# Kernel optimization log

Measured on AMD Instinct MI355X. Metric: run time of the kernel, lower is better.

Reference implementation:

```python
import jax, jax.numpy as jnp
import numpy as np

B, L, H, N, O = 64, 512, 768, 50, 768
ALPHA = 0.3  # leaky relu slope in GAT
NEG_INF = -9e15


def _position_encoding(n, d):
    # standard sinusoidal PE, shape [n, d]
    pos = jnp.arange(n, dtype=jnp.float32)[:, None]              # [n,1]
    div = jnp.exp(jnp.arange(0, d, 2, dtype=jnp.float32) * (-np.log(10000.0) / d))  # [d/2]
    ang = pos * div[None, :]                                     # [n, d/2]
    return jnp.stack([jnp.sin(ang), jnp.cos(ang)], axis=-1).reshape(n, d)


def _gat_layer(x, adj, W, b, a, ab):
    # Dense GAT layer. Original builds an [N,N,2F] concat tensor then applies
    # linear a; mathematically identical to splitting a into src/dst halves.
    Wh = x @ W + b                                               # [N,F]
    Fdim = Wh.shape[-1]
    a_src = Wh @ a[:Fdim]                                        # [N]
    a_dst = Wh @ a[Fdim:]                                        # [N]
    e = jax.nn.leaky_relu(a_src[:, None] + a_dst[None, :] + ab, negative_slope=ALPHA)
    att = jax.nn.softmax(jnp.where(adj > 0, e, NEG_INF), axis=1)  # rows sum to 1
    return att @ Wh                                              # [N,F]


def setup_inputs() -> dict:
    key = jax.random.key(0)
    ks = jax.random.split(key, 16)
    s = 1.0 / np.sqrt(H)
    utter_embedding = jax.random.normal(ks[0], (B, L, H), jnp.float32)
    cls_ids = jnp.sort(jax.random.randint(ks[1], (B, N), 0, L), axis=1).astype(jnp.int32)
    adj = jax.random.randint(ks[2], (B, N, N), 0, 2).astype(jnp.int32)
    adj = adj | jnp.eye(N, dtype=jnp.int32)  # ensure self loops so softmax rows are valid
    return {
        "utter_embedding": utter_embedding,
        "cls_ids": cls_ids,
        "adj": adj,
        # GAT head 0 (concat=True)
        "W1": jax.random.normal(ks[3], (H, H), jnp.float32) * s,
        "b1": jnp.zeros((H,), jnp.float32),
        "a1": jax.random.normal(ks[4], (2 * H,), jnp.float32) * s,
        "ab1": jnp.zeros((), jnp.float32),
        # GAT out layer (concat=False)
        "W2": jax.random.normal(ks[5], (H, H), jnp.float32) * s,
        "b2": jnp.zeros((H,), jnp.float32),
        "a2": jax.random.normal(ks[6], (2 * H,), jnp.float32) * s,
        "ab2": jnp.zeros((), jnp.float32),
        # Attention pooling over utterances
        "Wa": jax.random.normal(ks[7], (H, H), jnp.float32) * s,
        "ba": jnp.zeros((H,), jnp.float32),
        "v": jax.random.normal(ks[8], (H,), jnp.float32) * s,
        # Final linear
        "Wl": jax.random.normal(ks[9], (H, O), jnp.float32) * s,
        "bl": jnp.zeros((O,), jnp.float32),
    }


def reference(utter_embedding, cls_ids, adj, W1, b1, a1, ab1, W2, b2, a2, ab2,
              Wa, ba, v, Wl, bl):
    pe = _position_encoding(N, H)                                # [N,H]

    def per_dialogue(emb, ids, A):
        # gather [CLS] utterance embeddings: index_select
        x = jnp.take(emb, ids, axis=0)                           # [N,H]
        x = x + pe                                               # position encoder
        # GAT: 1 head concat -> elu, out layer -> elu, residual
        h = jax.nn.elu(_gat_layer(x, A, W1, b1, a1, ab1))
        h = jax.nn.elu(_gat_layer(h, A, W2, b2, a2, ab2)) + x    # residual per GAT.forward
        # attention pooling over N utterances
        scores = jax.nn.softmax(jnp.tanh(h @ Wa + ba) @ v, axis=0)  # [N]
        return scores @ h                                        # [H]

    dialogue = jax.vmap(per_dialogue)(utter_embedding, cls_ids, adj)  # [B,H]
    return dialogue @ Wl + bl                                    # [B,O]
```

## Files before the change

### kernel.cpp

```cpp
#include <hip/hip_runtime.h>
#include <hip/hip_bf16.h>
#include <math.h>

typedef __attribute__((ext_vector_type(8))) short bf16x8;
typedef __attribute__((ext_vector_type(4))) float f32x4;

constexpr int Bn = 64;
constexpr int Ln = 512;
constexpr int Hd = 768;
constexpr int Nn = 50;
constexpr int On = 768;

struct PrepArgs {
  const float* src[4];
  __hip_bfloat16* dst[4];
  float* aux;
  int auxn;
};

__global__ __launch_bounds__(256) void prep_kernel(PrepArgs args) {
  int job = blockIdx.y;
  if (job < 4) {
    __shared__ float tile[32][33];
    int t = blockIdx.x;
    int bx = (t % 24) * 32, by = (t / 24) * 32;
    const float* W = args.src[job];
    __hip_bfloat16* Wt = args.dst[job];
    int c = threadIdx.x & 31, r0 = threadIdx.x >> 5;
    for (int r = r0; r < 32; r += 8)
      tile[r][c] = W[(size_t)(bx + r) * Hd + by + c];
    __syncthreads();
    for (int r = r0; r < 32; r += 8)
      Wt[(size_t)(by + r) * Hd + bx + c] = __float2bfloat16(tile[c][r]);
  } else {
    int idx = blockIdx.x * 256 + threadIdx.x;
    if (idx < args.auxn) args.aux[idx] = 0.f;
  }
}

__global__ __launch_bounds__(256) void gather_pe_kernel(
    const float* __restrict__ emb, const int* __restrict__ ids,
    float* __restrict__ xf, __hip_bfloat16* __restrict__ xb) {
  int bn = blockIdx.x;
  int b = bn / Nn, n = bn % Nn;
  int id = ids[bn];
  const float* src = emb + ((size_t)b * Ln + id) * Hd;
  float* xo = xf + (size_t)bn * Hd;
  __hip_bfloat16* xbo = xb + (size_t)bn * Hd;
  const float kLog = 9.210340371976184f / (float)Hd;
  for (int h = threadIdx.x; h < Hd; h += 256) {
    int he = h & ~1;
    float freq = expf(-(float)he * kLog);
    float ang = (float)n * freq;
    float pe = (h & 1) ? cosf(ang) : sinf(ang);
    float v = src[h] + pe;
    xo[h] = v;
    xbo[h] = __float2bfloat16(v);
  }
}

template <int EPI>
__global__ __launch_bounds__(256) void gemm_kernel(
    const __hip_bfloat16* __restrict__ A, const __hip_bfloat16* __restrict__ Bt,
    const float* __restrict__ bias, float* __restrict__ C,
    const float* __restrict__ avec, float* __restrict__ o1,
    float* __restrict__ o2) {
  __shared__ __hip_bfloat16 As[64][40];
  __shared__ __hip_bfloat16 Bs[64][40];
  int tid = threadIdx.x;
  int wave = tid >> 6, lane = tid & 63;
  int lr = lane & 15, lq = lane >> 4;
  int row0 = blockIdx.x * 64, col0 = blockIdx.y * 64;
  int sr = tid >> 2, sk = (tid & 3) * 8;
  const __hip_bfloat16* Ap = A + (size_t)(row0 + sr) * Hd + sk;
  const __hip_bfloat16* Bp = Bt + (size_t)(col0 + sr) * Hd + sk;
  f32x4 acc[4] = {};
  for (int kt = 0; kt < Hd; kt += 32) {
    *(uint4*)&As[sr][sk] = *(const uint4*)(Ap + kt);
    *(uint4*)&Bs[sr][sk] = *(const uint4*)(Bp + kt);
    __syncthreads();
    bf16x8 af = *(const bf16x8*)&As[wave * 16 + lr][lq * 8];
#pragma unroll
    for (int ct = 0; ct < 4; ++ct) {
      bf16x8 bfrag = *(const bf16x8*)&Bs[ct * 16 + lr][lq * 8];
      acc[ct] = __builtin_amdgcn_mfma_f32_16x16x32_bf16(af, bfrag, acc[ct], 0, 0, 0);
    }
    __syncthreads();
  }
  int cr0 = row0 + wave * 16 + lq * 4;
  if (EPI == 0) {
    float ps[4] = {}, pd[4] = {};
#pragma unroll
    for (int ct = 0; ct < 4; ++ct) {
      int gc = col0 + ct * 16 + lr;
      float bv = bias[gc];
      float as_ = avec[gc], ad_ = avec[Hd + gc];
#pragma unroll
      for (int r = 0; r < 4; ++r) {
        float v = acc[ct][r] + bv;
        C[(size_t)(cr0 + r) * Hd + gc] = v;
        ps[r] += v * as_;
        pd[r] += v * ad_;
      }
    }
#pragma unroll
    for (int off = 8; off; off >>= 1)
#pragma unroll
      for (int r = 0; r < 4; ++r) {
        ps[r] += __shfl_xor(ps[r], off);
        pd[r] += __shfl_xor(pd[r], off);
      }
    if (lr == 0)
#pragma unroll
      for (int r = 0; r < 4; ++r) {
        atomicAdd(&o1[cr0 + r], ps[r]);
        atomicAdd(&o2[cr0 + r], pd[r]);
      }
  } else {
    float pr[4] = {};
#pragma unroll
    for (int ct = 0; ct < 4; ++ct) {
      int gc = col0 + ct * 16 + lr;
      float bv = bias[gc];
      float vv_ = avec[gc];
#pragma unroll
      for (int r = 0; r < 4; ++r) {
        float t = tanhf(acc[ct][r] + bv);
        pr[r] += t * vv_;
      }
    }
#pragma unroll
    for (int off = 8; off; off >>= 1)
#pragma unroll
      for (int r = 0; r < 4; ++r) pr[r] += __shfl_xor(pr[r], off);
    if (lr == 0)
#pragma unroll
      for (int r = 0; r < 4; ++r) atomicAdd(&o1[cr0 + r], pr[r]);
  }
}

template <int LAYER>
__global__ __launch_bounds__(256) void attf_kernel(
    const float* __restrict__ ssrc, const float* __restrict__ sdst,
    const int* __restrict__ adj, const float* __restrict__ ab,
    const float* __restrict__ Wh, const float* __restrict__ xres,
    float* __restrict__ hf, __hip_bfloat16* __restrict__ hb) {
  int b = blockIdx.y, h0 = blockIdx.x * 128;
  __shared__ float attL[Nn * Nn];
  float abv = ab[0];
  for (int idx = threadIdx.x; idx < Nn * Nn; idx += 256) {
    int i = idx / Nn, j = idx - i * Nn;
    float t = ssrc[b * Nn + i] + sdst[b * Nn + j] + abv;
    t = t > 0.f ? t : 0.3f * t;
    attL[idx] = (adj[(size_t)b * Nn * Nn + idx] > 0) ? t : -9.0e15f;
  }
  __syncthreads();
  if (threadIdx.x < Nn) {
    int i = threadIdx.x;
    float m = -3.0e38f;
    for (int j = 0; j < Nn; ++j) m = fmaxf(m, attL[i * Nn + j]);
    float s = 0.f;
    for (int j = 0; j < Nn; ++j) {
      float p = expf(attL[i * Nn + j] - m);
      attL[i * Nn + j] = p;
      s += p;
    }
    float inv = 1.f / s;
    for (int j = 0; j < Nn; ++j) attL[i * Nn + j] *= inv;
  }
  __syncthreads();
  int col = threadIdx.x & 127, half = threadIdx.x >> 7;
  int i0 = half * 25;
  float acc[25] = {};
  const float* Whb = Wh + ((size_t)b * Nn) * Hd + h0 + col;
  for (int j = 0; j < Nn; j += 2) {
    float w0 = Whb[(size_t)j * Hd];
    float w1 = Whb[(size_t)(j + 1) * Hd];
#pragma unroll
    for (int ii = 0; ii < 25; ++ii) {
      float2 a2 = *(const float2*)&attL[(i0 + ii) * Nn + j];
      acc[ii] += a2.x * w0 + a2.y * w1;
    }
  }
#pragma unroll
  for (int ii = 0; ii < 25; ++ii) {
    float v = acc[ii];
    v = v > 0.f ? v : expf(v) - 1.f;
    size_t off = ((size_t)b * Nn + i0 + ii) * Hd + h0 + col;
    if (LAYER == 2) {
      v += xres[off];
      hf[off] = v;
    }
    hb[off] = __float2bfloat16(v);
  }
}

__global__ __launch_bounds__(256) void poolfinal_kernel(
    const float* __restrict__ sraw, const float* __restrict__ h2,
    const __hip_bfloat16* __restrict__ Wlt, const float* __restrict__ bl,
    float* __restrict__ out) {
  int b = blockIdx.x;
  __shared__ float sc[Nn];
  __shared__ float ds[Hd];
  if (threadIdx.x < 64) {
    int j = threadIdx.x;
    float e = (j < Nn) ? sraw[b * Nn + j] : -3.0e38f;
    float m = e;
#pragma unroll
    for (int off = 32; off; off >>= 1) m = fmaxf(m, __shfl_xor(m, off));
    float p = (j < Nn) ? expf(e - m) : 0.f;
    float s = p;
#pragma unroll
    for (int off = 32; off; off >>= 1) s += __shfl_xor(s, off);
    if (j < Nn) sc[j] = p / s;
  }
  __syncthreads();
  for (int h = threadIdx.x; h < Hd; h += 256) {
    float a = 0.f;
#pragma unroll 10
    for (int j = 0; j < Nn; ++j) a += sc[j] * h2[((size_t)b * Nn + j) * Hd + h];
    ds[h] = a;
  }
  __syncthreads();
  for (int oo = 0; oo < 3; ++oo) {
    int o = oo * 256 + threadIdx.x;
    float acc = bl[o];
    const uint4* wr = (const uint4*)(Wlt + (size_t)o * Hd);
    for (int kk = 0; kk < Hd / 8; ++kk) {
      union { uint4 u; unsigned short s[8]; } w;
      w.u = wr[kk];
#pragma unroll
      for (int t = 0; t < 8; ++t)
        acc += ds[kk * 8 + t] * __uint_as_float((unsigned)w.s[t] << 16);
    }
    out[(size_t)b * On + o] = acc;
  }
}

extern "C" void kernel_launch(void* const* d_in, const int* in_sizes, int n_in,
                              void* d_out, int out_size, void* d_ws, size_t ws_size,
                              hipStream_t stream) {
  const float* emb = (const float*)d_in[0];
  const int* ids = (const int*)d_in[1];
  const int* adj = (const int*)d_in[2];
  const float* W1 = (const float*)d_in[3];
  const float* b1 = (const float*)d_in[4];
  const float* a1 = (const float*)d_in[5];
  const float* ab1 = (const float*)d_in[6];
  const float* W2 = (const float*)d_in[7];
  const float* b2 = (const float*)d_in[8];
  const float* a2 = (const float*)d_in[9];
  const float* ab2 = (const float*)d_in[10];
  const float* Wa = (const float*)d_in[11];
  const float* ba = (const float*)d_in[12];
  const float* vv = (const float*)d_in[13];
  const float* Wl = (const float*)d_in[14];
  const float* bl = (const float*)d_in[15];
  float* out = (float*)d_out;

  char* p = (char*)d_ws;
  auto alloc = [&](size_t bytes) {
    char* r = p;
    p += (bytes + 255) & ~(size_t)255;
    return r;
  };
  __hip_bfloat16* Wt1 = (__hip_bfloat16*)alloc((size_t)Hd * Hd * 2);
  __hip_bfloat16* Wt2 = (__hip_bfloat16*)alloc((size_t)Hd * Hd * 2);
  __hip_bfloat16* Wta = (__hip_bfloat16*)alloc((size_t)Hd * Hd * 2);
  __hip_bfloat16* Wlt = (__hip_bfloat16*)alloc((size_t)Hd * On * 2);
  float* aux = (float*)alloc(5 * Bn * Nn * 4);
  float* ssrc1 = aux;
  float* sdst1 = aux + Bn * Nn;
  float* ssrc2 = aux + 2 * Bn * Nn;
  float* sdst2 = aux + 3 * Bn * Nn;
  float* sraw = aux + 4 * Bn * Nn;
  float* xf = (float*)alloc((size_t)Bn * Nn * Hd * 4);
  __hip_bfloat16* xb = (__hip_bfloat16*)alloc((size_t)Bn * Nn * Hd * 2);
  float* Wh = (float*)alloc((size_t)Bn * Nn * Hd * 4);
  float* h2f = (float*)alloc((size_t)Bn * Nn * Hd * 4);
  __hip_bfloat16* hb = (__hip_bfloat16*)alloc((size_t)Bn * Nn * Hd * 2);

  PrepArgs pa;
  pa.src[0] = W1; pa.src[1] = W2; pa.src[2] = Wa; pa.src[3] = Wl;
  pa.dst[0] = Wt1; pa.dst[1] = Wt2; pa.dst[2] = Wta; pa.dst[3] = Wlt;
  pa.aux = aux; pa.auxn = 5 * Bn * Nn;
  prep_kernel<<<dim3(576, 5), 256, 0, stream>>>(pa);

  gather_pe_kernel<<<Bn * Nn, 256, 0, stream>>>(emb, ids, xf, xb);

  dim3 ggrid(Bn * Nn / 64, Hd / 64);
  dim3 agrid(Hd / 128, Bn);

  gemm_kernel<0><<<ggrid, 256, 0, stream>>>(xb, Wt1, b1, Wh, a1, ssrc1, sdst1);
  attf_kernel<1><<<agrid, 256, 0, stream>>>(ssrc1, sdst1, adj, ab1, Wh,
                                            nullptr, nullptr, hb);
  gemm_kernel<0><<<ggrid, 256, 0, stream>>>(hb, Wt2, b2, Wh, a2, ssrc2, sdst2);
  attf_kernel<2><<<agrid, 256, 0, stream>>>(ssrc2, sdst2, adj, ab2, Wh,
                                            xf, h2f, hb);
  gemm_kernel<1><<<ggrid, 256, 0, stream>>>(hb, Wta, ba, nullptr, vv, sraw,
                                            nullptr);
  poolfinal_kernel<<<Bn, 256, 0, stream>>>(sraw, h2f, Wlt, bl, out);
}
```

Baseline: 313.3 us.

## Double-buffer GEMM LDS, store Wh in bf16, merge gather into prep kernel

The GEMM main loop now uses two LDS buffers. The next k-tile is loaded into registers while MFMAs run on the current tile, which removes one barrier per iteration. The intermediate Wh is stored as bf16 instead of fp32, halving its write and read traffic in the GEMM epilogue and the attention kernel, at some precision cost. The gather/position-encoding kernel is folded into the prep kernel to save one launch, and the attention grid is flattened to 1D.

```diff
diff --git a/kernel.cpp b/kernel.cpp
--- a/kernel.cpp
+++ b/kernel.cpp
@@ -14,59 +14,59 @@
 struct PrepArgs {
   const float* src[4];
   __hip_bfloat16* dst[4];
+  const float* emb;
+  const int* ids;
+  float* xf;
+  __hip_bfloat16* xb;
   float* aux;
   int auxn;
 };
 
-__global__ __launch_bounds__(256) void prep_kernel(PrepArgs args) {
-  int job = blockIdx.y;
-  if (job < 4) {
-    __shared__ float tile[32][33];
-    int t = blockIdx.x;
-    int bx = (t % 24) * 32, by = (t / 24) * 32;
-    const float* W = args.src[job];
-    __hip_bfloat16* Wt = args.dst[job];
+__global__ __launch_bounds__(256) void prep_kernel(PrepArgs a) {
+  __shared__ float tile[32][33];
+  int bx = blockIdx.x;
+  if (bx < 2304) {
+    int job = bx / 576, t = bx % 576;
+    const float* W = a.src[job];
+    __hip_bfloat16* Wt = a.dst[job];
+    int tx = (t % 24) * 32, ty = (t / 24) * 32;
     int c = threadIdx.x & 31, r0 = threadIdx.x >> 5;
     for (int r = r0; r < 32; r += 8)
-      tile[r][c] = W[(size_t)(bx + r) * Hd + by + c];
+      tile[r][c] = W[(size_t)(tx + r) * Hd + ty + c];
     __syncthreads();
     for (int r = r0; r < 32; r += 8)
-      Wt[(size_t)(by + r) * Hd + bx + c] = __float2bfloat16(tile[c][r]);
+      Wt[(size_t)(ty + r) * Hd + tx + c] = __float2bfloat16(tile[c][r]);
+  } else if (bx < 5504) {
+    int bn = bx - 2304;
+    int b = bn / Nn, n = bn % Nn;
+    int id = a.ids[bn];
+    const float* src = a.emb + ((size_t)b * Ln + id) * Hd;
+    float* xo = a.xf + (size_t)bn * Hd;
+    __hip_bfloat16* xbo = a.xb + (size_t)bn * Hd;
+    const float kLog = 9.210340371976184f / (float)Hd;
+    for (int h = threadIdx.x; h < Hd; h += 256) {
+      int he = h & ~1;
+      float freq = expf(-(float)he * kLog);
+      float ang = (float)n * freq;
+      float pe = (h & 1) ? cosf(ang) : sinf(ang);
+      float v = src[h] + pe;
+      xo[h] = v;
+      xbo[h] = __float2bfloat16(v);
+    }
   } else {
-    int idx = blockIdx.x * 256 + threadIdx.x;
-    if (idx < args.auxn) args.aux[idx] = 0.f;
-  }
-}
-
-__global__ __launch_bounds__(256) void gather_pe_kernel(
-    const float* __restrict__ emb, const int* __restrict__ ids,
-    float* __restrict__ xf, __hip_bfloat16* __restrict__ xb) {
-  int bn = blockIdx.x;
-  int b = bn / Nn, n = bn % Nn;
-  int id = ids[bn];
-  const float* src = emb + ((size_t)b * Ln + id) * Hd;
-  float* xo = xf + (size_t)bn * Hd;
-  __hip_bfloat16* xbo = xb + (size_t)bn * Hd;
-  const float kLog = 9.210340371976184f / (float)Hd;
-  for (int h = threadIdx.x; h < Hd; h += 256) {
-    int he = h & ~1;
-    float freq = expf(-(float)he * kLog);
-    float ang = (float)n * freq;
-    float pe = (h & 1) ? cosf(ang) : sinf(ang);
-    float v = src[h] + pe;
-    xo[h] = v;
-    xbo[h] = __float2bfloat16(v);
+    int idx = (bx - 5504) * 256 + threadIdx.x;
+    if (idx < a.auxn) a.aux[idx] = 0.f;
   }
 }
 
 template <int EPI>
 __global__ __launch_bounds__(256) void gemm_kernel(
     const __hip_bfloat16* __restrict__ A, const __hip_bfloat16* __restrict__ Bt,
-    const float* __restrict__ bias, float* __restrict__ C,
+    const float* __restrict__ bias, __hip_bfloat16* __restrict__ C,
     const float* __restrict__ avec, float* __restrict__ o1,
     float* __restrict__ o2) {
-  __shared__ __hip_bfloat16 As[64][40];
-  __shared__ __hip_bfloat16 Bs[64][40];
+  __shared__ __hip_bfloat16 As[2][64][40];
+  __shared__ __hip_bfloat16 Bs[2][64][40];
   int tid = threadIdx.x;
   int wave = tid >> 6, lane = tid & 63;
   int lr = lane & 15, lq = lane >> 4;
@@ -74,18 +74,34 @@
   int sr = tid >> 2, sk = (tid & 3) * 8;
   const __hip_bfloat16* Ap = A + (size_t)(row0 + sr) * Hd + sk;
   const __hip_bfloat16* Bp = Bt + (size_t)(col0 + sr) * Hd + sk;
+  uint4 ra = *(const uint4*)Ap;
+  uint4 rb = *(const uint4*)Bp;
+  *(uint4*)&As[0][sr][sk] = ra;
+  *(uint4*)&Bs[0][sr][sk] = rb;
   f32x4 acc[4] = {};
-  for (int kt = 0; kt < Hd; kt += 32) {
-    *(uint4*)&As[sr][sk] = *(const uint4*)(Ap + kt);
-    *(uint4*)&Bs[sr][sk] = *(const uint4*)(Bp + kt);
+  __syncthreads();
+  int cur = 0;
+  for (int kt = 32; kt < Hd; kt += 32) {
+    ra = *(const uint4*)(Ap + kt);
+    rb = *(const uint4*)(Bp + kt);
+    bf16x8 af = *(const bf16x8*)&As[cur][wave * 16 + lr][lq * 8];
+#pragma unroll
+    for (int ct = 0; ct < 4; ++ct) {
+      bf16x8 bfrag = *(const bf16x8*)&Bs[cur][ct * 16 + lr][lq * 8];
+      acc[ct] = __builtin_amdgcn_mfma_f32_16x16x32_bf16(af, bfrag, acc[ct], 0, 0, 0);
+    }
+    *(uint4*)&As[cur ^ 1][sr][sk] = ra;
+    *(uint4*)&Bs[cur ^ 1][sr][sk] = rb;
     __syncthreads();
-    bf16x8 af = *(const bf16x8*)&As[wave * 16 + lr][lq * 8];
+    cur ^= 1;
+  }
+  {
+    bf16x8 af = *(const bf16x8*)&As[cur][wave * 16 + lr][lq * 8];
 #pragma unroll
     for (int ct = 0; ct < 4; ++ct) {
-      bf16x8 bfrag = *(const bf16x8*)&Bs[ct * 16 + lr][lq * 8];
+      bf16x8 bfrag = *(const bf16x8*)&Bs[cur][ct * 16 + lr][lq * 8];
       acc[ct] = __builtin_amdgcn_mfma_f32_16x16x32_bf16(af, bfrag, acc[ct], 0, 0, 0);
     }
-    __syncthreads();
   }
   int cr0 = row0 + wave * 16 + lq * 4;
   if (EPI == 0) {
@@ -98,7 +114,7 @@
 #pragma unroll
       for (int r = 0; r < 4; ++r) {
         float v = acc[ct][r] + bv;
-        C[(size_t)(cr0 + r) * Hd + gc] = v;
+        C[(size_t)(cr0 + r) * Hd + gc] = __float2bfloat16(v);
         ps[r] += v * as_;
         pd[r] += v * ad_;
       }
@@ -143,9 +159,9 @@
 __global__ __launch_bounds__(256) void attf_kernel(
     const float* __restrict__ ssrc, const float* __restrict__ sdst,
     const int* __restrict__ adj, const float* __restrict__ ab,
-    const float* __restrict__ Wh, const float* __restrict__ xres,
+    const __hip_bfloat16* __restrict__ Wh, const float* __restrict__ xres,
     float* __restrict__ hf, __hip_bfloat16* __restrict__ hb) {
-  int b = blockIdx.y, h0 = blockIdx.x * 128;
+  int b = blockIdx.x / 6, h0 = (blockIdx.x % 6) * 128;
   __shared__ float attL[Nn * Nn];
   float abv = ab[0];
   for (int idx = threadIdx.x; idx < Nn * Nn; idx += 256) {
@@ -172,10 +188,10 @@
   int col = threadIdx.x & 127, half = threadIdx.x >> 7;
   int i0 = half * 25;
   float acc[25] = {};
-  const float* Whb = Wh + ((size_t)b * Nn) * Hd + h0 + col;
+  const __hip_bfloat16* Whb = Wh + ((size_t)b * Nn) * Hd + h0 + col;
   for (int j = 0; j < Nn; j += 2) {
-    float w0 = Whb[(size_t)j * Hd];
-    float w1 = Whb[(size_t)(j + 1) * Hd];
+    float w0 = __bfloat162float(Whb[(size_t)j * Hd]);
+    float w1 = __bfloat162float(Whb[(size_t)(j + 1) * Hd]);
 #pragma unroll
     for (int ii = 0; ii < 25; ++ii) {
       float2 a2 = *(const float2*)&attL[(i0 + ii) * Nn + j];
@@ -276,27 +292,28 @@
   float* sraw = aux + 4 * Bn * Nn;
   float* xf = (float*)alloc((size_t)Bn * Nn * Hd * 4);
   __hip_bfloat16* xb = (__hip_bfloat16*)alloc((size_t)Bn * Nn * Hd * 2);
-  float* Wh = (float*)alloc((size_t)Bn * Nn * Hd * 4);
+  __hip_bfloat16* Whb16 = (__hip_bfloat16*)alloc((size_t)Bn * Nn * Hd * 2);
   float* h2f = (float*)alloc((size_t)Bn * Nn * Hd * 4);
   __hip_bfloat16* hb = (__hip_bfloat16*)alloc((size_t)Bn * Nn * Hd * 2);
 
   PrepArgs pa;
   pa.src[0] = W1; pa.src[1] = W2; pa.src[2] = Wa; pa.src[3] = Wl;
   pa.dst[0] = Wt1; pa.dst[1] = Wt2; pa.dst[2] = Wta; pa.dst[3] = Wlt;
+  pa.emb = emb; pa.ids = ids; pa.xf = xf; pa.xb = xb;
   pa.aux = aux; pa.auxn = 5 * Bn * Nn;
-  prep_kernel<<<dim3(576, 5), 256, 0, stream>>>(pa);
-
-  gather_pe_kernel<<<Bn * Nn, 256, 0, stream>>>(emb, ids, xf, xb);
+  prep_kernel<<<5567, 256, 0, stream>>>(pa);
 
   dim3 ggrid(Bn * Nn / 64, Hd / 64);
-  dim3 agrid(Hd / 128, Bn);
-
-  gemm_kernel<0><<<ggrid, 256, 0, stream>>>(xb, Wt1, b1, Wh, a1, ssrc1, sdst1);
-  attf_kernel<1><<<agrid, 256, 0, stream>>>(ssrc1, sdst1, adj, ab1, Wh,
+  dim3 agrid(6 * Bn);
+
+  gemm_kernel<0><<<ggrid, 256, 0, stream>>>(xb, Wt1, b1, Whb16, a1, ssrc1,
+                                            sdst1);
+  attf_kernel<1><<<agrid, 256, 0, stream>>>(ssrc1, sdst1, adj, ab1, Whb16,
                                             nullptr, nullptr, hb);
-  gemm_kernel<0><<<ggrid, 256, 0, stream>>>(hb, Wt2, b2, Wh, a2, ssrc2, sdst2);
-  attf_kernel<2><<<agrid, 256, 0, stream>>>(ssrc2, sdst2, adj, ab2, Wh,
-                                            xf, h2f, hb);
+  gemm_kernel<0><<<ggrid, 256, 0, stream>>>(hb, Wt2, b2, Whb16, a2, ssrc2,
+                                            sdst2);
+  attf_kernel<2><<<agrid, 256, 0, stream>>>(ssrc2, sdst2, adj, ab2, Whb16, xf,
+                                            h2f, hb);
   gemm_kernel<1><<<ggrid, 256, 0, stream>>>(hb, Wta, ba, nullptr, vv, sraw,
                                             nullptr);
   poolfinal_kernel<<<Bn, 256, 0, stream>>>(sraw, h2f, Wlt, bl, out);
```

Result: faster. 305.8 us (-2.4%).

## Fuse entire GAT pipeline into one persistent per-dialogue kernel

Applied to the files above, without the earlier changes.

Replaces the gather, three GEMM, two attention and pooling kernels with a single 768-thread kernel per dialogue. Each block runs all phases, using MFMA for both the dense GEMMs and the attention-times-Wh step through a bf16 transposed Wh buffer padded to 64 rows. Intermediates are stored as bf16 and reductions are kept in shared memory, which removes launch overhead, fp32 intermediate traffic and global atomics. The cost is only 64 blocks on the device, with each block streaming the full weight matrices straight from global or L2 without LDS tiling. The final linear layer also no longer transposes Wl and reads it column-wise.

```diff
diff --git a/kernel.cpp b/kernel.cpp
--- a/kernel.cpp
+++ b/kernel.cpp
@@ -4,300 +4,296 @@
 
 typedef __attribute__((ext_vector_type(8))) short bf16x8;
 typedef __attribute__((ext_vector_type(4))) float f32x4;
+typedef __attribute__((ext_vector_type(4))) unsigned short u16x4;
 
 constexpr int Bn = 64;
 constexpr int Ln = 512;
 constexpr int Hd = 768;
 constexpr int Nn = 50;
 constexpr int On = 768;
-
-struct PrepArgs {
-  const float* src[4];
-  __hip_bfloat16* dst[4];
-  float* aux;
-  int auxn;
-};
-
-__global__ __launch_bounds__(256) void prep_kernel(PrepArgs args) {
-  int job = blockIdx.y;
-  if (job < 4) {
+constexpr int RP = 64;
+
+__device__ __forceinline__ f32x4 MFMA(bf16x8 a, bf16x8 b, f32x4 c) {
+  return __builtin_amdgcn_mfma_f32_16x16x32_bf16(a, b, c, 0, 0, 0);
+}
+__device__ __forceinline__ unsigned short f2bb(float v) {
+  __hip_bfloat16 h = __float2bfloat16(v);
+  return *(unsigned short*)&h;
+}
+
+struct PrepArgs { const float* src[4]; __hip_bfloat16* dst[4]; };
+
+__global__ __launch_bounds__(256) void prep_kernel(PrepArgs a) {
+  int bx = blockIdx.x;
+  int job = bx / 576, t = bx % 576;
+  if (job < 3) {
     __shared__ float tile[32][33];
-    int t = blockIdx.x;
-    int bx = (t % 24) * 32, by = (t / 24) * 32;
-    const float* W = args.src[job];
-    __hip_bfloat16* Wt = args.dst[job];
+    const float* W = a.src[job];
+    __hip_bfloat16* Wt = a.dst[job];
+    int tx = (t % 24) * 32, ty = (t / 24) * 32;
     int c = threadIdx.x & 31, r0 = threadIdx.x >> 5;
     for (int r = r0; r < 32; r += 8)
-      tile[r][c] = W[(size_t)(bx + r) * Hd + by + c];
+      tile[r][c] = W[(size_t)(tx + r) * Hd + ty + c];
     __syncthreads();
     for (int r = r0; r < 32; r += 8)
-      Wt[(size_t)(by + r) * Hd + bx + c] = __float2bfloat16(tile[c][r]);
+      Wt[(size_t)(ty + r) * Hd + tx + c] = __float2bfloat16(tile[c][r]);
   } else {
-    int idx = blockIdx.x * 256 + threadIdx.x;
-    if (idx < args.auxn) args.aux[idx] = 0.f;
-  }
-}
-
-__global__ __launch_bounds__(256) void gather_pe_kernel(
-    const float* __restrict__ emb, const int* __restrict__ ids,
-    float* __restrict__ xf, __hip_bfloat16* __restrict__ xb) {
-  int bn = blockIdx.x;
-  int b = bn / Nn, n = bn % Nn;
-  int id = ids[bn];
-  const float* src = emb + ((size_t)b * Ln + id) * Hd;
-  float* xo = xf + (size_t)bn * Hd;
-  __hip_bfloat16* xbo = xb + (size_t)bn * Hd;
-  const float kLog = 9.210340371976184f / (float)Hd;
-  for (int h = threadIdx.x; h < Hd; h += 256) {
-    int he = h & ~1;
-    float freq = expf(-(float)he * kLog);
-    float ang = (float)n * freq;
-    float pe = (h & 1) ? cosf(ang) : sinf(ang);
-    float v = src[h] + pe;
-    xo[h] = v;
-    xbo[h] = __float2bfloat16(v);
-  }
-}
-
-template <int EPI>
-__global__ __launch_bounds__(256) void gemm_kernel(
-    const __hip_bfloat16* __restrict__ A, const __hip_bfloat16* __restrict__ Bt,
-    const float* __restrict__ bias, float* __restrict__ C,
-    const float* __restrict__ avec, float* __restrict__ o1,
-    float* __restrict__ o2) {
-  __shared__ __hip_bfloat16 As[64][40];
-  __shared__ __hip_bfloat16 Bs[64][40];
-  int tid = threadIdx.x;
-  int wave = tid >> 6, lane = tid & 63;
-  int lr = lane & 15, lq = lane >> 4;
-  int row0 = blockIdx.x * 64, col0 = blockIdx.y * 64;
-  int sr = tid >> 2, sk = (tid & 3) * 8;
-  const __hip_bfloat16* Ap = A + (size_t)(row0 + sr) * Hd + sk;
-  const __hip_bfloat16* Bp = Bt + (size_t)(col0 + sr) * Hd + sk;
-  f32x4 acc[4] = {};
-  for (int kt = 0; kt < Hd; kt += 32) {
-    *(uint4*)&As[sr][sk] = *(const uint4*)(Ap + kt);
-    *(uint4*)&Bs[sr][sk] = *(const uint4*)(Bp + kt);
-    __syncthreads();
-    bf16x8 af = *(const bf16x8*)&As[wave * 16 + lr][lq * 8];
-#pragma unroll
-    for (int ct = 0; ct < 4; ++ct) {
-      bf16x8 bfrag = *(const bf16x8*)&Bs[ct * 16 + lr][lq * 8];
-      acc[ct] = __builtin_amdgcn_mfma_f32_16x16x32_bf16(af, bfrag, acc[ct], 0, 0, 0);
-    }
-    __syncthreads();
-  }
-  int cr0 = row0 + wave * 16 + lq * 4;
-  if (EPI == 0) {
-    float ps[4] = {}, pd[4] = {};
-#pragma unroll
-    for (int ct = 0; ct < 4; ++ct) {
-      int gc = col0 + ct * 16 + lr;
+    const float* W = a.src[3];
+    __hip_bfloat16* D = a.dst[3];
+    int base = t * 1024 + threadIdx.x;
+#pragma unroll
+    for (int k = 0; k < 4; ++k) {
+      int idx = base + k * 256;
+      D[idx] = __float2bfloat16(W[idx]);
+    }
+  }
+}
+
+struct MainArgs {
+  const float* emb; const int* ids; const int* adj;
+  const float *b1, *a1, *ab1, *b2, *a2, *ab2, *ba, *vv, *bl;
+  const __hip_bfloat16 *Wt1, *Wt2, *Wta, *Wlb;
+  __hip_bfloat16 *xb, *h1, *h2, *WhT1, *WhT2;
+  float* xres;
+  float* out;
+};
+
+__global__ __launch_bounds__(768) void main_kernel(MainArgs A) {
+  __shared__ float attL[Nn * 52];
+  __shared__ __hip_bfloat16 attB[64 * 72];
+  __shared__ float ssrcP[64], sdstP[64], srawP[64], sc[64], ds[Hd];
+
+  const int b = blockIdx.x;
+  const int tid = threadIdx.x;
+  const int w = tid >> 6, lane = tid & 63, lr = lane & 15, lq = lane >> 4;
+  const int rt = w & 3, cg = w >> 2;
+  const int cr0 = rt * 16 + lq * 4;
+
+  __hip_bfloat16* xb = A.xb + (size_t)b * RP * Hd;
+  __hip_bfloat16* h1 = A.h1 + (size_t)b * RP * Hd;
+  __hip_bfloat16* h2 = A.h2 + (size_t)b * RP * Hd;
+  __hip_bfloat16* WhT1 = A.WhT1 + (size_t)b * Hd * RP;
+  __hip_bfloat16* WhT2 = A.WhT2 + (size_t)b * Hd * RP;
+  float* xres = A.xres + (size_t)b * RP * Hd;
+
+  for (int i = tid; i < 64 * 72; i += 768) attB[i] = __float2bfloat16(0.f);
+  if (tid < 64) { ssrcP[tid] = 0.f; sdstP[tid] = 0.f; srawP[tid] = 0.f; }
+  {
+    const float kLog = 9.210340371976184f / (float)Hd;
+    float freq = expf(-(float)(tid & ~1) * kLog);
+    for (int i = 0; i < Nn; ++i) {
+      int id = A.ids[b * Nn + i];
+      float v = A.emb[((size_t)b * Ln + id) * Hd + tid];
+      float ang = (float)i * freq;
+      v += (tid & 1) ? cosf(ang) : sinf(ang);
+      xb[(size_t)i * Hd + tid] = __float2bfloat16(v);
+      xres[(size_t)i * Hd + tid] = v;
+    }
+    for (int i = Nn; i < RP; ++i) {
+      xb[(size_t)i * Hd + tid] = __float2bfloat16(0.f);
+      xres[(size_t)i * Hd + tid] = 0.f;
+    }
+  }
+  __syncthreads();
+
+  auto gemm_phase = [&](const __hip_bfloat16* Ag, const __hip_bfloat16* Wt,
+                        const float* bias, const float* avec,
+                        __hip_bfloat16* WhT, float* o1, float* o2, int EPI) {
+    const __hip_bfloat16* Ap = Ag + (size_t)(rt * 16 + lr) * Hd + lq * 8;
+    const __hip_bfloat16* Bp0 = Wt + (size_t)(cg * 256 + lr) * Hd + lq * 8;
+    f32x4 acc[16] = {};
+    for (int kt = 0; kt < Hd; kt += 32) {
+      bf16x8 af = *(const bf16x8*)(Ap + kt);
+      const __hip_bfloat16* Bp = Bp0 + kt;
+#pragma unroll
+      for (int s = 0; s < 16; ++s)
+        acc[s] = MFMA(af, *(const bf16x8*)(Bp + (size_t)s * 16 * Hd), acc[s]);
+    }
+    float p1[4] = {}, p2[4] = {};
+#pragma unroll
+    for (int s = 0; s < 16; ++s) {
+      int gc = cg * 256 + s * 16 + lr;
       float bv = bias[gc];
-      float as_ = avec[gc], ad_ = avec[Hd + gc];
+      if (EPI == 0) {
+        float a_s = avec[gc], a_d = avec[Hd + gc];
+        u16x4 pk;
+#pragma unroll
+        for (int r = 0; r < 4; ++r) {
+          float v = acc[s][r] + bv;
+          pk[r] = f2bb(v);
+          p1[r] += v * a_s;
+          p2[r] += v * a_d;
+        }
+        *(u16x4*)(WhT + (size_t)gc * RP + cr0) = pk;
+      } else {
+        float vv_ = avec[gc];
+#pragma unroll
+        for (int r = 0; r < 4; ++r)
+          p1[r] += tanhf(acc[s][r] + bv) * vv_;
+      }
+    }
+#pragma unroll
+    for (int off = 8; off; off >>= 1)
 #pragma unroll
       for (int r = 0; r < 4; ++r) {
-        float v = acc[ct][r] + bv;
-        C[(size_t)(cr0 + r) * Hd + gc] = v;
-        ps[r] += v * as_;
-        pd[r] += v * ad_;
-      }
-    }
-#pragma unroll
-    for (int off = 8; off; off >>= 1)
+        p1[r] += __shfl_xor(p1[r], off);
+        if (EPI == 0) p2[r] += __shfl_xor(p2[r], off);
+      }
+    if (lr == 0)
 #pragma unroll
       for (int r = 0; r < 4; ++r) {
-        ps[r] += __shfl_xor(ps[r], off);
-        pd[r] += __shfl_xor(pd[r], off);
-      }
-    if (lr == 0)
+        int row = cr0 + r;
+        if (row < Nn) {
+          atomicAdd(&o1[row], p1[r]);
+          if (EPI == 0) atomicAdd(&o2[row], p2[r]);
+        }
+      }
+  };
+
+  auto att_phase = [&](const float* ab) {
+    float abv = ab[0];
+    for (int idx = tid; idx < Nn * Nn; idx += 768) {
+      int i = idx / Nn, j = idx - i * Nn;
+      float t = ssrcP[i] + sdstP[j] + abv;
+      t = t > 0.f ? t : 0.3f * t;
+      attL[i * 52 + j] = (A.adj[(size_t)b * Nn * Nn + idx] > 0) ? t : -9.0e15f;
+    }
+    __syncthreads();
+    if (tid < Nn) {
+      float m = -3.0e38f;
+      for (int j = 0; j < Nn; ++j) m = fmaxf(m, attL[tid * 52 + j]);
+      float s = 0.f;
+      for (int j = 0; j < Nn; ++j) {
+        float p = expf(attL[tid * 52 + j] - m);
+        attL[tid * 52 + j] = p;
+        s += p;
+      }
+      float inv = 1.f / s;
+      for (int j = 0; j < Nn; ++j) attL[tid * 52 + j] *= inv;
+    } else if (tid >= 128 && tid < 192) {
+      ssrcP[tid - 128] = 0.f;
+      sdstP[tid - 128] = 0.f;
+    }
+    __syncthreads();
+    for (int idx = tid; idx < Nn * Nn; idx += 768) {
+      int i = idx / Nn, j = idx - i * Nn;
+      attB[i * 72 + j] = __float2bfloat16(attL[i * 52 + j]);
+    }
+    __syncthreads();
+  };
+
+  auto attwh_phase = [&](const __hip_bfloat16* WhT, __hip_bfloat16* Hout,
+                         int LAYER) {
+    bf16x8 a0 = *(const bf16x8*)&attB[(rt * 16 + lr) * 72 + lq * 8];
+    bf16x8 a1 = *(const bf16x8*)&attB[(rt * 16 + lr) * 72 + 32 + lq * 8];
+#pragma unroll
+    for (int s = 0; s < 16; ++s) {
+      int gc = cg * 256 + s * 16 + lr;
+      const __hip_bfloat16* Bp = WhT + (size_t)gc * RP + lq * 8;
+      f32x4 acc = {};
+      acc = MFMA(a0, *(const bf16x8*)Bp, acc);
+      acc = MFMA(a1, *(const bf16x8*)(Bp + 32), acc);
 #pragma unroll
       for (int r = 0; r < 4; ++r) {
-        atomicAdd(&o1[cr0 + r], ps[r]);
-        atomicAdd(&o2[cr0 + r], pd[r]);
-      }
-  } else {
-    float pr[4] = {};
-#pragma unroll
-    for (int ct = 0; ct < 4; ++ct) {
-      int gc = col0 + ct * 16 + lr;
-      float bv = bias[gc];
-      float vv_ = avec[gc];
-#pragma unroll
-      for (int r = 0; r < 4; ++r) {
-        float t = tanhf(acc[ct][r] + bv);
-        pr[r] += t * vv_;
-      }
-    }
-#pragma unroll
-    for (int off = 8; off; off >>= 1)
-#pragma unroll
-      for (int r = 0; r < 4; ++r) pr[r] += __shfl_xor(pr[r], off);
-    if (lr == 0)
-#pragma unroll
-      for (int r = 0; r < 4; ++r) atomicAdd(&o1[cr0 + r], pr[r]);
-  }
-}
-
-template <int LAYER>
-__global__ __launch_bounds__(256) void attf_kernel(
-    const float* __restrict__ ssrc, const float* __restrict__ sdst,
-    const int* __restrict__ adj, const float* __restrict__ ab,
-    const float* __restrict__ Wh, const float* __restrict__ xres,
-    float* __restrict__ hf, __hip_bfloat16* __restrict__ hb) {
-  int b = blockIdx.y, h0 = blockIdx.x * 128;
-  __shared__ float attL[Nn * Nn];
-  float abv = ab[0];
-  for (int idx = threadIdx.x; idx < Nn * Nn; idx += 256) {
-    int i = idx / Nn, j = idx - i * Nn;
-    float t = ssrc[b * Nn + i] + sdst[b * Nn + j] + abv;
-    t = t > 0.f ? t : 0.3f * t;
-    attL[idx] = (adj[(size_t)b * Nn * Nn + idx] > 0) ? t : -9.0e15f;
-  }
-  __syncthreads();
-  if (threadIdx.x < Nn) {
-    int i = threadIdx.x;
-    float m = -3.0e38f;
-    for (int j = 0; j < Nn; ++j) m = fmaxf(m, attL[i * Nn + j]);
-    float s = 0.f;
-    for (int j = 0; j < Nn; ++j) {
-      float p = expf(attL[i * Nn + j] - m);
-      attL[i * Nn + j] = p;
-      s += p;
-    }
-    float inv = 1.f / s;
-    for (int j = 0; j < Nn; ++j) attL[i * Nn + j] *= inv;
-  }
-  __syncthreads();
-  int col = threadIdx.x & 127, half = threadIdx.x >> 7;
-  int i0 = half * 25;
-  float acc[25] = {};
-  const float* Whb = Wh + ((size_t)b * Nn) * Hd + h0 + col;
-  for (int j = 0; j < Nn; j += 2) {
-    float w0 = Whb[(size_t)j * Hd];
-    float w1 = Whb[(size_t)(j + 1) * Hd];
-#pragma unroll
-    for (int ii = 0; ii < 25; ++ii) {
-      float2 a2 = *(const float2*)&attL[(i0 + ii) * Nn + j];
-      acc[ii] += a2.x * w0 + a2.y * w1;
-    }
-  }
-#pragma unroll
-  for (int ii = 0; ii < 25; ++ii) {
-    float v = acc[ii];
-    v = v > 0.f ? v : expf(v) - 1.f;
-    size_t off = ((size_t)b * Nn + i0 + ii) * Hd + h0 + col;
-    if (LAYER == 2) {
-      v += xres[off];
-      hf[off] = v;
-    }
-    hb[off] = __float2bfloat16(v);
-  }
-}
-
-__global__ __launch_bounds__(256) void poolfinal_kernel(
-    const float* __restrict__ sraw, const float* __restrict__ h2,
-    const __hip_bfloat16* __restrict__ Wlt, const float* __restrict__ bl,
-    float* __restrict__ out) {
-  int b = blockIdx.x;
-  __shared__ float sc[Nn];
-  __shared__ float ds[Hd];
-  if (threadIdx.x < 64) {
-    int j = threadIdx.x;
-    float e = (j < Nn) ? sraw[b * Nn + j] : -3.0e38f;
+        float v = acc[r];
+        v = v > 0.f ? v : expf(v) - 1.f;
+        size_t off = (size_t)(cr0 + r) * Hd + gc;
+        if (LAYER == 2) v += xres[off];
+        Hout[off] = __float2bfloat16(v);
+      }
+    }
+  };
+
+  gemm_phase(xb, A.Wt1, A.b1, A.a1, WhT1, ssrcP, sdstP, 0);
+  __syncthreads();
+  att_phase(A.ab1);
+  attwh_phase(WhT1, h1, 1);
+  __syncthreads();
+
+  gemm_phase(h1, A.Wt2, A.b2, A.a2, WhT2, ssrcP, sdstP, 0);
+  __syncthreads();
+  att_phase(A.ab2);
+  attwh_phase(WhT2, h2, 2);
+  __syncthreads();
+
+  gemm_phase(h2, A.Wta, A.ba, A.vv, nullptr, srawP, nullptr, 1);
+  __syncthreads();
+
+  if (tid < 64) {
+    float e = (tid < Nn) ? srawP[tid] : -3.0e38f;
     float m = e;
 #pragma unroll
     for (int off = 32; off; off >>= 1) m = fmaxf(m, __shfl_xor(m, off));
-    float p = (j < Nn) ? expf(e - m) : 0.f;
+    float p = (tid < Nn) ? expf(e - m) : 0.f;
     float s = p;
 #pragma unroll
     for (int off = 32; off; off >>= 1) s += __shfl_xor(s, off);
-    if (j < Nn) sc[j] = p / s;
-  }
-  __syncthreads();
-  for (int h = threadIdx.x; h < Hd; h += 256) {
+    if (tid < Nn) sc[tid] = p / s;
+  }
+  __syncthreads();
+  {
     float a = 0.f;
 #pragma unroll 10
-    for (int j = 0; j < Nn; ++j) a += sc[j] * h2[((size_t)b * Nn + j) * Hd + h];
-    ds[h] = a;
-  }
-  __syncthreads();
-  for (int oo = 0; oo < 3; ++oo) {
-    int o = oo * 256 + threadIdx.x;
-    float acc = bl[o];
-    const uint4* wr = (const uint4*)(Wlt + (size_t)o * Hd);
-    for (int kk = 0; kk < Hd / 8; ++kk) {
-      union { uint4 u; unsigned short s[8]; } w;
-      w.u = wr[kk];
-#pragma unroll
-      for (int t = 0; t < 8; ++t)
-        acc += ds[kk * 8 + t] * __uint_as_float((unsigned)w.s[t] << 16);
-    }
-    out[(size_t)b * On + o] = acc;
+    for (int j = 0; j < Nn; ++j)
+      a += sc[j] * __bfloat162float(h2[(size_t)j * Hd + tid]);
+    ds[tid] = a;
+  }
+  __syncthreads();
+
+  {
+    float acc = A.bl[tid];
+    const __hip_bfloat16* Wc = A.Wlb + tid;
+#pragma unroll 8
+    for (int k = 0; k < Hd; ++k)
+      acc += ds[k] * __bfloat162float(Wc[(size_t)k * Hd]);
+    A.out[(size_t)b * On + tid] = acc;
   }
 }
 
 extern "C" void kernel_launch(void* const* d_in, const int* in_sizes, int n_in,
                               void* d_out, int out_size, void* d_ws, size_t ws_size,
                               hipStream_t stream) {
-  const float* emb = (const float*)d_in[0];
-  const int* ids = (const int*)d_in[1];
-  const int* adj = (const int*)d_in[2];
-  const float* W1 = (const float*)d_in[3];
-  const float* b1 = (const float*)d_in[4];
-  const float* a1 = (const float*)d_in[5];
-  const float* ab1 = (const float*)d_in[6];
-  const float* W2 = (const float*)d_in[7];
-  const float* b2 = (const float*)d_in[8];
-  const float* a2 = (const float*)d_in[9];
-  const float* ab2 = (const float*)d_in[10];
-  const float* Wa = (const float*)d_in[11];
-  const float* ba = (const float*)d_in[12];
-  const float* vv = (const float*)d_in[13];
-  const float* Wl = (const float*)d_in[14];
-  const float* bl = (const float*)d_in[15];
-  float* out = (float*)d_out;
-
   char* p = (char*)d_ws;
   auto alloc = [&](size_t bytes) {
     char* r = p;
     p += (bytes + 255) & ~(size_t)255;
     return r;
   };
+  MainArgs a;
+  a.emb = (const float*)d_in[0];
+  a.ids = (const int*)d_in[1];
+  a.adj = (const int*)d_in[2];
+  const float* W1 = (const float*)d_in[3];
+  a.b1 = (const float*)d_in[4];
+  a.a1 = (const float*)d_in[5];
+  a.ab1 = (const float*)d_in[6];
+  const float* W2 = (const float*)d_in[7];
+  a.b2 = (const float*)d_in[8];
+  a.a2 = (const float*)d_in[9];
+  a.ab2 = (const float*)d_in[10];
+  const float* Wa = (const float*)d_in[11];
+  a.ba = (const float*)d_in[12];
+  a.vv = (const float*)d_in[13];
+  const float* Wl = (const float*)d_in[14];
+  a.bl = (const float*)d_in[15];
+  a.out = (float*)d_out;
+
   __hip_bfloat16* Wt1 = (__hip_bfloat16*)alloc((size_t)Hd * Hd * 2);
   __hip_bfloat16* Wt2 = (__hip_bfloat16*)alloc((size_t)Hd * Hd * 2);
   __hip_bfloat16* Wta = (__hip_bfloat16*)alloc((size_t)Hd * Hd * 2);
-  __hip_bfloat16* Wlt = (__hip_bfloat16*)alloc((size_t)Hd * On * 2);
-  float* aux = (float*)alloc(5 * Bn * Nn * 4);
-  float* ssrc1 = aux;
-  float* sdst1 = aux + Bn * Nn;
-  float* ssrc2 = aux + 2 * Bn * Nn;
-  float* sdst2 = aux + 3 * Bn * Nn;
-  float* sraw = aux + 4 * Bn * Nn;
-  float* xf = (float*)alloc((size_t)Bn * Nn * Hd * 4);
-  __hip_bfloat16* xb = (__hip_bfloat16*)alloc((size_t)Bn * Nn * Hd * 2);
-  float* Wh = (float*)alloc((size_t)Bn * Nn * Hd * 4);
-  float* h2f = (float*)alloc((size_t)Bn * Nn * Hd * 4);
-  __hip_bfloat16* hb = (__hip_bfloat16*)alloc((size_t)Bn * Nn * Hd * 2);
+  __hip_bfloat16* Wlb = (__hip_bfloat16*)alloc((size_t)Hd * On * 2);
+  a.Wt1 = Wt1; a.Wt2 = Wt2; a.Wta = Wta; a.Wlb = Wlb;
+  a.xb = (__hip_bfloat16*)alloc((size_t)Bn * RP * Hd * 2);
+  a.h1 = (__hip_bfloat16*)alloc((size_t)Bn * RP * Hd * 2);
+  a.h2 = (__hip_bfloat16*)alloc((size_t)Bn * RP * Hd * 2);
+  a.WhT1 = (__hip_bfloat16*)alloc((size_t)Bn * Hd * RP * 2);
+  a.WhT2 = (__hip_bfloat16*)alloc((size_t)Bn * Hd * RP * 2);
+  a.xres = (float*)alloc((size_t)Bn * RP * Hd * 4);
 
   PrepArgs pa;
   pa.src[0] = W1; pa.src[1] = W2; pa.src[2] = Wa; pa.src[3] = Wl;
-  pa.dst[0] = Wt1; pa.dst[1] = Wt2; pa.dst[2] = Wta; pa.dst[3] = Wlt;
-  pa.aux = aux; pa.auxn = 5 * Bn * Nn;
-  prep_kernel<<<dim3(576, 5), 256, 0, stream>>>(pa);
-
-  gather_pe_kernel<<<Bn * Nn, 256, 0, stream>>>(emb, ids, xf, xb);
-
-  dim3 ggrid(Bn * Nn / 64, Hd / 64);
-  dim3 agrid(Hd / 128, Bn);
-
-  gemm_kernel<0><<<ggrid, 256, 0, stream>>>(xb, Wt1, b1, Wh, a1, ssrc1, sdst1);
-  attf_kernel<1><<<agrid, 256, 0, stream>>>(ssrc1, sdst1, adj, ab1, Wh,
-                                            nullptr, nullptr, hb);
-  gemm_kernel<0><<<ggrid, 256, 0, stream>>>(hb, Wt2, b2, Wh, a2, ssrc2, sdst2);
-  attf_kernel<2><<<agrid, 256, 0, stream>>>(ssrc2, sdst2, adj, ab2, Wh,
-                                            xf, h2f, hb);
-  gemm_kernel<1><<<ggrid, 256, 0, stream>>>(hb, Wta, ba, nullptr, vv, sraw,
-                                            nullptr);
-  poolfinal_kernel<<<Bn, 256, 0, stream>>>(sraw, h2f, Wlt, bl, out);
-}
+  pa.dst[0] = Wt1; pa.dst[1] = Wt2; pa.dst[2] = Wta; pa.dst[3] = Wlb;
+  prep_kernel<<<4 * 576, 256, 0, stream>>>(pa);
+
+  main_kernel<<<Bn, 768, 0, stream>>>(a);
+}
```

Measured after the change: 711.3 us. 127% more time.
